# Optimization experiments

Hardware: AMD Instinct MI355X
Metric: run time of the kernel (lower is better)

Reference implementation:

```python
import jax, jax.numpy as jnp
import numpy as np

D_MODEL = 2048
NUM_HEADS = 16
D_K = D_MODEL // NUM_HEADS


def _xavier(key, shape):
    # xavier_uniform_ for a (fan_in, fan_out) matrix
    limit = np.sqrt(6.0 / (shape[0] + shape[1]))
    return jax.random.uniform(key, shape, dtype=jnp.float32, minval=-limit, maxval=limit)


def setup_inputs() -> dict:
    key = jax.random.key(0)
    kx, kq, kk, kv, ko = jax.random.split(key, 5)
    x = jax.random.normal(kx, (4, 2048, D_MODEL), dtype=jnp.float32)
    return {
        "x": x,
        "w_q": _xavier(kq, (D_MODEL, D_MODEL)),
        "w_k": _xavier(kk, (D_MODEL, D_MODEL)),
        "w_v": _xavier(kv, (D_MODEL, D_MODEL)),
        "w_o": _xavier(ko, (D_MODEL, D_MODEL)),
    }


def _split_heads(t):
    b, s, _ = t.shape
    return t.reshape(b, s, NUM_HEADS, D_K).transpose(0, 2, 1, 3)  # [b,h,s,dk]


def reference(x, w_q, w_k, w_v, w_o):
    q = _split_heads(x @ w_q)
    k = _split_heads(x @ w_k)
    v = _split_heads(x @ w_v)
    scale = 1.0 / np.sqrt(D_K).astype(np.float32)
    scores = jnp.einsum("bhqd,bhkd->bhqk", q, k) * scale
    attn = jax.nn.softmax(scores, axis=-1)
    out = jnp.einsum("bhqk,bhkd->bhqd", attn, v)  # [b,h,s,dk]
    b, h, s, dk = out.shape
    out = out.transpose(0, 2, 1, 3).reshape(b, s, h * dk)
    return out @ w_o
```

## Files before the change

kernel.cpp:

```cpp
#include <hip/hip_runtime.h>
#include <hip/hip_bf16.h>

typedef __attribute__((ext_vector_type(8))) __bf16 bf16x8;
typedef __attribute__((ext_vector_type(4))) __bf16 bf16x4;
typedef __attribute__((ext_vector_type(4))) float f32x4;
typedef __attribute__((ext_vector_type(16))) float f32x16;
typedef __attribute__((ext_vector_type(8))) unsigned short u16x8;
typedef unsigned short u16;

#define DEVINL static __device__ __forceinline__

namespace {
constexpr int kB = 4;
constexpr int kS = 2048;
constexpr int kDM = 2048;
constexpr int kH = 16;
constexpr int kDK = 128;
constexpr int kM = kB * kS;
constexpr int kNQKV = 3 * kDM;
constexpr float kE2 = 0.08838834764831845f * 1.44269504088896f;
}

DEVINL u16 f2bf(float f) {
  __hip_bfloat16 h = __float2bfloat16(f);
  return __builtin_bit_cast(u16, h);
}

#if __has_builtin(__builtin_amdgcn_exp2f)
DEVINL float exp2_fast(float x) { return __builtin_amdgcn_exp2f(x); }
#else
DEVINL float exp2_fast(float x) { return exp2f(x); }
#endif

#define GLOAD16(gp, lp) \
  __builtin_amdgcn_global_load_lds((const __attribute__((address_space(1))) void*)(gp), \
                                   (__attribute__((address_space(3))) void*)(lp), 16, 0, 0)

DEVINL bf16x8 lds_frag(const u16* p) { return *reinterpret_cast<const bf16x8*>(p); }

DEVINL f32x4 MFMA16x16(bf16x8 a, bf16x8 b, f32x4 c) {
  return __builtin_amdgcn_mfma_f32_16x16x32_bf16(a, b, c, 0, 0, 0);
}

struct TrueT { static constexpr bool value = true; };
struct FalseT { static constexpr bool value = false; };

__global__ __launch_bounds__(256) void cast_x_kernel(const float* __restrict__ x,
                                                     u16* __restrict__ o, int n4) {
  int i = blockIdx.x * 256 + threadIdx.x;
  if (i >= n4) return;
  float4 v = reinterpret_cast<const float4*>(x)[i];
  ushort4 r;
  r.x = f2bf(v.x); r.y = f2bf(v.y); r.z = f2bf(v.z); r.w = f2bf(v.w);
  reinterpret_cast<ushort4*>(o)[i] = r;
}

__global__ __launch_bounds__(256) void transpose_w_kernel(const float* __restrict__ w0,
    const float* __restrict__ w1, const float* __restrict__ w2, const float* __restrict__ w3,
    u16* __restrict__ wtcat, u16* __restrict__ wot) {
  const float* src = (blockIdx.z == 0) ? w0 : (blockIdx.z == 1) ? w1
                    : (blockIdx.z == 2) ? w2 : w3;
  u16* dst = (blockIdx.z < 3) ? (wtcat + (size_t)blockIdx.z * kDM * kDM) : wot;
  __shared__ float tile[32][33];
  int n0 = blockIdx.x * 32, k0 = blockIdx.y * 32;
  int tx = threadIdx.x, ty = threadIdx.y;
#pragma unroll
  for (int i = 0; i < 4; ++i)
    tile[ty + i * 8][tx] = src[(size_t)(k0 + ty + i * 8) * kDM + n0 + tx];
  __syncthreads();
#pragma unroll
  for (int i = 0; i < 4; ++i)
    dst[(size_t)(n0 + ty + i * 8) * kDM + k0 + tx] = f2bf(tile[tx][ty + i * 8]);
}

__global__ __launch_bounds__(256) void transpose_v_kernel(const u16* __restrict__ qkv,
                                                          u16* __restrict__ vt) {
  int bh = blockIdx.z, b = bh >> 4, h = bh & 15;
  int s0 = blockIdx.x * 32, d0 = blockIdx.y * 32;
  __shared__ u16 tile[32][33];
  int tx = threadIdx.x, ty = threadIdx.y;
#pragma unroll
  for (int i = 0; i < 4; ++i)
    tile[ty + i * 8][tx] =
        qkv[(size_t)(b * kS + s0 + ty + i * 8) * kNQKV + 2 * kDM + h * kDK + d0 + tx];
  __syncthreads();
#pragma unroll
  for (int i = 0; i < 4; ++i)
    vt[(size_t)(bh * kDK + d0 + ty + i * 8) * kS + s0 + tx] = tile[tx][ty + i * 8];
}

DEVINL void cstore(float* p, float v) { *p = v; }
DEVINL void cstore(u16* p, float v) { *p = f2bf(v); }

#define BAR_MID()                                      \
  __builtin_amdgcn_sched_barrier(0);                   \
  __builtin_amdgcn_s_barrier();                        \
  asm volatile("s_waitcnt lgkmcnt(0)" ::: "memory");   \
  __builtin_amdgcn_sched_barrier(0);                   \
  __builtin_amdgcn_s_setprio(1)

#define BAR_END()                                      \
  __builtin_amdgcn_s_setprio(0);                       \
  __builtin_amdgcn_sched_barrier(0);                   \
  __builtin_amdgcn_s_barrier()

#define LGK8() asm volatile("s_waitcnt lgkmcnt(8)" ::: "memory")

#define RD_A(SB, MQ)                                                  \
  do {                                                                \
    _Pragma("unroll") for (int mf = 0; mf < 4; ++mf) {                \
      const u16* p_ = (SB) + (awrow + (MQ) * 64 + mf * 16) * 64;      \
      a[mf * 2 + 0] = lds_frag(p_ + g0);                              \
      a[mf * 2 + 1] = lds_frag(p_ + g1);                              \
    }                                                                 \
  } while (0)

#define RD_B(SB, NH)                                                  \
  do {                                                                \
    _Pragma("unroll") for (int nf = 0; nf < 2; ++nf) {                \
      const u16* p_ = (SB) + (bwrow + (NH) * 32 + nf * 16) * 64;      \
      b[(NH) * 4 + nf * 2 + 0] = lds_frag(p_ + g0);                   \
      b[(NH) * 4 + nf * 2 + 1] = lds_frag(p_ + g1);                   \
    }                                                                 \
  } while (0)

#define MM16(MQ, NH)                                                  \
  do {                                                                \
    _Pragma("unroll") for (int mf = 0; mf < 4; ++mf)                  \
      _Pragma("unroll") for (int nf = 0; nf < 2; ++nf) {              \
        f32x4 t_ = acc[(MQ) * 4 + mf][(NH) * 2 + nf];                 \
        t_ = MFMA16x16(a[mf * 2 + 0], b[(NH) * 4 + nf * 2 + 0], t_);  \
        t_ = MFMA16x16(a[mf * 2 + 1], b[(NH) * 4 + nf * 2 + 1], t_);  \
        acc[(MQ) * 4 + mf][(NH) * 2 + nf] = t_;                       \
      }                                                               \
  } while (0)

#define STG_A(buf, R0, kt) \
  GLOAD16(baseA + (size_t)(R0) * lda + (size_t)(kt) * 64, ldsA + (buf) * 16384 + (R0) * 64)
#define STG_B(buf, R0, kt) \
  GLOAD16(baseB + (size_t)(R0) * ldb + (size_t)(kt) * 64, ldsB + (buf) * 16384 + (R0) * 64)

template <typename CT>
__global__ __launch_bounds__(512, 2) void gemm256_kernel(const u16* __restrict__ A,
    const u16* __restrict__ Bt, CT* __restrict__ C, int K, int lda, int ldb, int ldc) {
  __shared__ __align__(16) u16 sA[2][16384];
  __shared__ __align__(16) u16 sB[2][16384];
  const int tid = threadIdx.x;
  const int lane = tid & 63, wid = tid >> 6;
  const int r15 = lane & 15, hi = lane >> 4;
  const int wm = wid >> 2, wn = wid & 3;

  const int gx = gridDim.x, nwg = gx * gridDim.y;
  const int orig = blockIdx.y * gx + blockIdx.x;
  const int wg = (orig & 7) * (nwg >> 3) + (orig >> 3);
  const int n0 = (wg % gx) * 256;
  const int m0 = (wg / gx) * 256;

  const int NT = K >> 6;
  const int NITER = NT >> 1;

  const int rc = tid >> 3;
  const int cg = (tid & 7) ^ (rc & 7);
  const u16* baseA = A + (size_t)(m0 + rc) * lda + cg * 8;
  const u16* baseB = Bt + (size_t)(n0 + rc) * ldb + cg * 8;
  u16* ldsA = &sA[0][0] + rc * 64 + (tid & 7) * 8;
  u16* ldsB = &sB[0][0] + rc * 64 + (tid & 7) * 8;

  const int sw = r15 & 7;
  const int g0 = (hi ^ sw) * 8;
  const int g1 = ((4 + hi) ^ sw) * 8;
  const int awrow = wm * 128 + r15;
  const int bwrow = wn * 64 + r15;
  const u16* sA0 = &sA[0][0]; const u16* sA1 = &sA[1][0];
  const u16* sB0 = &sB[0][0]; const u16* sB1 = &sB[1][0];

  f32x4 acc[8][4] = {};
  bf16x8 a[8], b[8];

  STG_A(0, 0, 0); STG_A(0, 64, 0); STG_A(0, 128, 0); STG_A(0, 192, 0);
  STG_B(0, 0, 0); STG_B(0, 64, 0); STG_B(0, 128, 0); STG_B(0, 192, 0);
  STG_A(1, 0, 1); STG_A(1, 128, 1);
  STG_B(1, 0, 1); STG_B(1, 64, 1); STG_B(1, 128, 1); STG_B(1, 192, 1);
  asm volatile("s_waitcnt vmcnt(6)" ::: "memory");
  __builtin_amdgcn_sched_barrier(0);
  __builtin_amdgcn_s_barrier();

  int kb = 0;
  auto iter = [&](auto lastc) {
    constexpr bool L = decltype(lastc)::value;
    const int kO = kb + 1, k2 = kb + 2, k3 = kb + 3;
    RD_A(sA0, 0); RD_B(sB0, 0);
    STG_A(1, 64, kO); STG_A(1, 192, kO);
    LGK8(); BAR_MID(); MM16(0, 0); BAR_END();
    RD_B(sB0, 1);
    if constexpr (!L) { STG_A(0, 0, k2); STG_A(0, 128, k2); }
    BAR_MID(); MM16(0, 1); BAR_END();
    RD_A(sA0, 1);
    if constexpr (!L) { STG_B(0, 0, k2); STG_B(0, 64, k2); }
    BAR_MID(); MM16(1, 0); BAR_END();
    if constexpr (!L) { STG_B(0, 128, k2); STG_B(0, 192, k2); }
    BAR_MID(); MM16(1, 1);
    __builtin_amdgcn_s_setprio(0);
    if constexpr (L) { asm volatile("s_waitcnt vmcnt(0)" ::: "memory"); }
    else             { asm volatile("s_waitcnt vmcnt(6)" ::: "memory"); }
    __builtin_amdgcn_sched_barrier(0);
    __builtin_amdgcn_s_barrier();
    RD_A(sA1, 0); RD_B(sB1, 0);
    if constexpr (!L) { STG_A(0, 64, k2); STG_A(0, 192, k2); }
    LGK8(); BAR_MID(); MM16(0, 0); BAR_END();
    RD_B(sB1, 1);
    if constexpr (!L) { STG_A(1, 0, k3); STG_A(1, 128, k3); }
    BAR_MID(); MM16(0, 1); BAR_END();
    RD_A(sA1, 1);
    if constexpr (!L) { STG_B(1, 0, k3); STG_B(1, 64, k3); }
    BAR_MID(); MM16(1, 0); BAR_END();
    if constexpr (!L) { STG_B(1, 128, k3); STG_B(1, 192, k3); }
    BAR_MID(); MM16(1, 1);
    __builtin_amdgcn_s_setprio(0);
    if constexpr (L) { asm volatile("s_waitcnt vmcnt(0)" ::: "memory"); }
    else             { asm volatile("s_waitcnt vmcnt(6)" ::: "memory"); }
    __builtin_amdgcn_sched_barrier(0);
    __builtin_amdgcn_s_barrier();
    kb += 2;
  };
  for (int i = 0; i < NITER - 1; ++i) iter(FalseT{});
  iter(TrueT{});

  const size_t crow0 = (size_t)(m0 + wm * 128 + hi * 4);
  const int col0 = n0 + wn * 64 + r15;
#pragma unroll
  for (int im = 0; im < 8; ++im)
#pragma unroll
    for (int in = 0; in < 4; ++in)
#pragma unroll
      for (int r = 0; r < 4; ++r)
        cstore(&C[(crow0 + im * 16 + r) * ldc + col0 + in * 16], acc[im][in][r]);
}

__global__ __launch_bounds__(256, 2) void attn_kernel(const u16* __restrict__ qkv,
    const u16* __restrict__ vt, u16* __restrict__ attn_out) {
  __shared__ __align__(16) u16 lds[2][16384];
  const int tid = threadIdx.x;
  const int lane = tid & 63, wid = tid >> 6;
  const int l31 = lane & 31, hi5 = lane >> 5;
  const int q0 = blockIdx.x * 128, h = blockIdx.y, b = blockIdx.z;
  const int bh = b * kH + h;

  const int krow = tid >> 4, kg = tid & 15;
  const u16* kp = qkv + (size_t)(b * kS + krow) * kNQKV + kDM + h * kDK
                  + (size_t)((kg ^ (krow & 7)) * 8);
  const int vrow = tid >> 3, vg = tid & 7;
  const u16* vp = vt + (size_t)(bh * kDK + vrow) * kS + (size_t)((vg ^ (vrow & 7)) * 8);

  auto stage_kv = [&](u16* dst) {
#pragma unroll
    for (int i = 0; i < 4; ++i)
      GLOAD16(kp + (size_t)i * 16 * kNQKV, dst + (tid + 256 * i) * 8);
#pragma unroll
    for (int i = 0; i < 4; ++i)
      GLOAD16(vp + (size_t)i * 32 * kS, dst + 8192 + (tid + 256 * i) * 8);
    kp += (size_t)64 * kNQKV;
    vp += 64;
  };

#pragma unroll
  for (int i = 0; i < 8; ++i) {
    int row = (tid >> 4) + 16 * i;
    GLOAD16(qkv + (size_t)(b * kS + q0 + row) * kNQKV + h * kDK
                + (size_t)(((tid & 15) ^ (row & 7)) * 8),
            (u16*)lds[1] + (tid + 256 * i) * 8);
  }
  stage_kv(lds[0]);
  __syncthreads();

  bf16x8 qf[8];
  {
    const int qrow = wid * 32 + l31;
    const u16* qb = (const u16*)lds[1];
#pragma unroll
    for (int ds = 0; ds < 8; ++ds) {
      int slot = (ds * 2 + hi5) ^ (qrow & 7);
      qf[ds] = lds_frag(&qb[qrow * 128 + slot * 8]);
    }
  }
  __syncthreads();

  f32x16 o[4] = {};
  float mi = -1e30f, li = 0.f;
  int cur = 0;

  for (int t = 0; t < kS / 64; ++t) {
    if (t < kS / 64 - 1) stage_kv(lds[cur ^ 1]);

    const u16* Kb = (const u16*)lds[cur];
    const u16* Vb = Kb + 8192;

    f32x16 s0 = {}, s1 = {};
    const int kr = l31;
#pragma unroll
    for (int ds = 0; ds < 8; ++ds) {
      int slot = ((ds * 2 + hi5) ^ (kr & 7)) * 8;
      bf16x8 k0 = lds_frag(&Kb[kr * 128 + slot]);
      bf16x8 k1 = lds_frag(&Kb[(32 + kr) * 128 + slot]);
      s0 = __builtin_amdgcn_mfma_f32_32x32x16_bf16(k0, qf[ds], s0, 0, 0, 0);
      s1 = __builtin_amdgcn_mfma_f32_32x32x16_bf16(k1, qf[ds], s1, 0, 0, 0);
    }

    float mx = s0[0];
#pragma unroll
    for (int r = 1; r < 16; ++r) mx = fmaxf(mx, s0[r]);
#pragma unroll
    for (int r = 0; r < 16; ++r) mx = fmaxf(mx, s1[r]);
    mx = fmaxf(mx, __shfl_xor(mx, 32));
    float mc = mx * kE2;
    if (__any(mc > mi + 8.0f)) {
      float mn = fmaxf(mi, mc);
      float corr = exp2_fast(mi - mn);
      mi = mn;
      li *= corr;
#pragma unroll
      for (int r = 0; r < 16; ++r) {
        float c = __shfl(corr, (r & 3) + 8 * (r >> 2) + 4 * hi5);
        o[0][r] *= c; o[1][r] *= c; o[2][r] *= c; o[3][r] *= c;
      }
    }
    float p0[16], p1[16];
    float rs = 0.f;
#pragma unroll
    for (int r = 0; r < 16; ++r) { p0[r] = exp2_fast(s0[r] * kE2 - mi); rs += p0[r]; }
#pragma unroll
    for (int r = 0; r < 16; ++r) { p1[r] = exp2_fast(s1[r] * kE2 - mi); rs += p1[r]; }
    rs += __shfl_xor(rs, 32);
    li += rs;

    u16x8 pw0, pw1, pw2, pw3;
#pragma unroll
    for (int r = 0; r < 8; ++r) {
      pw0[r] = f2bf(p0[r]);
      pw1[r] = f2bf(p0[r + 8]);
      pw2[r] = f2bf(p1[r]);
      pw3[r] = f2bf(p1[r + 8]);
    }
    bf16x8 pa[4] = {__builtin_bit_cast(bf16x8, pw0), __builtin_bit_cast(bf16x8, pw1),
                    __builtin_bit_cast(bf16x8, pw2), __builtin_bit_cast(bf16x8, pw3)};

#pragma unroll
    for (int dt = 0; dt < 4; ++dt) {
      const int row = dt * 32 + l31;
      const int rs8 = row & 7;
#pragma unroll
      for (int ks = 0; ks < 4; ++ks) {
        bf16x4 vlo = *reinterpret_cast<const bf16x4*>(
            &Vb[row * 64 + ((ks * 2) ^ rs8) * 8 + hi5 * 4]);
        bf16x4 vhi = *reinterpret_cast<const bf16x4*>(
            &Vb[row * 64 + ((ks * 2 + 1) ^ rs8) * 8 + hi5 * 4]);
        bf16x8 bv = __builtin_shufflevector(vlo, vhi, 0, 1, 2, 3, 4, 5, 6, 7);
        o[dt] = __builtin_amdgcn_mfma_f32_32x32x16_bf16(pa[ks], bv, o[dt], 0, 0, 0);
      }
    }

    __syncthreads();
    cur ^= 1;
  }

  float rli = 1.0f / li;
  const size_t obase = (size_t)(b * kS + q0 + wid * 32) * kDM + h * kDK + l31;
#pragma unroll
  for (int r = 0; r < 16; ++r) {
    int ql = (r & 3) + 8 * (r >> 2) + 4 * hi5;
    float w = __shfl(rli, ql);
#pragma unroll
    for (int dt = 0; dt < 4; ++dt)
      attn_out[obase + (size_t)ql * kDM + dt * 32] = f2bf(o[dt][r] * w);
  }
}

extern "C" void kernel_launch(void* const* d_in, const int* in_sizes, int n_in,
                              void* d_out, int out_size, void* d_ws, size_t ws_size,
                              hipStream_t stream) {
  (void)in_sizes; (void)n_in; (void)out_size; (void)ws_size;
  const float* x  = (const float*)d_in[0];
  const float* wq = (const float*)d_in[1];
  const float* wk = (const float*)d_in[2];
  const float* wv = (const float*)d_in[3];
  const float* wo = (const float*)d_in[4];

  char* p = (char*)d_ws;
  u16* xb   = (u16*)p; p += (size_t)kM * kDM * 2;
  u16* wtc  = (u16*)p; p += (size_t)kNQKV * kDM * 2;
  u16* wot  = (u16*)p; p += (size_t)kDM * kDM * 2;
  u16* qkvb = (u16*)p; p += (size_t)kM * kNQKV * 2;
  u16* vtb  = (u16*)p; p += (size_t)kB * kH * kDK * kS * 2;
  u16* aob  = xb;

  int n4 = kM * kDM / 4;
  cast_x_kernel<<<(n4 + 255) / 256, 256, 0, stream>>>(x, xb, n4);
  transpose_w_kernel<<<dim3(kDM / 32, kDM / 32, 4), dim3(32, 8), 0, stream>>>(
      wq, wk, wv, wo, wtc, wot);
  gemm256_kernel<u16><<<dim3(kNQKV / 256, kM / 256), 512, 0, stream>>>(
      xb, wtc, qkvb, kDM, kDM, kDM, kNQKV);
  transpose_v_kernel<<<dim3(kS / 32, kDK / 32, kB * kH), dim3(32, 8), 0, stream>>>(
      qkvb, vtb);
  attn_kernel<<<dim3(kS / 128, kH, kB), 256, 0, stream>>>(qkvb, vtb, aob);
  gemm256_kernel<float><<<dim3(kDM / 256, kM / 256), 512, 0, stream>>>(
      aob, wot, (float*)d_out, kDM, kDM, kDM, kDM);
}
```

Baseline: 460.4 us.

## Double-buffer A fragments in registers to overlap LDS reads with MFMA phases

Splits the A register fragments into even and odd sets so each phase issues the LDS reads for the next phase before running its own MFMAs. The first fragments are loaded before the loop, and the global-load wait moves earlier to allow this. The aim is to hide LDS read latency behind matrix math instead of stalling on lgkmcnt before each MFMA block. The extra fragment registers raise register pressure, which could reduce occupancy at launch bounds of 512 threads with 2 blocks, and the reordered waits and barriers risk ordering errors in the shared-memory buffers.

Result: no change. 460.3 us (-0.0%).

```diff
diff --git a/kernel.cpp b/kernel.cpp
--- a/kernel.cpp
+++ b/kernel.cpp
@@ -92,30 +92,42 @@
 DEVINL void cstore(float* p, float v) { *p = v; }
 DEVINL void cstore(u16* p, float v) { *p = f2bf(v); }
 
-#define BAR_MID()                                      \
+#define PH_OPEN()                                      \
   __builtin_amdgcn_sched_barrier(0);                   \
   __builtin_amdgcn_s_barrier();                        \
   asm volatile("s_waitcnt lgkmcnt(0)" ::: "memory");   \
   __builtin_amdgcn_sched_barrier(0);                   \
   __builtin_amdgcn_s_setprio(1)
 
-#define BAR_END()                                      \
+#define PH_CLOSE()                                     \
   __builtin_amdgcn_s_setprio(0);                       \
   __builtin_amdgcn_sched_barrier(0);                   \
   __builtin_amdgcn_s_barrier()
 
-#define LGK8() asm volatile("s_waitcnt lgkmcnt(8)" ::: "memory")
-
-#define RD_A(SB, MQ)                                                  \
+#define PH_CLOSE_G4()                                  \
+  __builtin_amdgcn_s_setprio(0);                       \
+  __builtin_amdgcn_sched_barrier(0);                   \
+  asm volatile("s_waitcnt vmcnt(4)" ::: "memory");     \
+  __builtin_amdgcn_sched_barrier(0);                   \
+  __builtin_amdgcn_s_barrier()
+
+#define PH_CLOSE_G0()                                  \
+  __builtin_amdgcn_s_setprio(0);                       \
+  __builtin_amdgcn_sched_barrier(0);                   \
+  asm volatile("s_waitcnt vmcnt(0)" ::: "memory");     \
+  __builtin_amdgcn_sched_barrier(0);                   \
+  __builtin_amdgcn_s_barrier()
+
+#define RD_A(SB, MQ, DST)                                             \
   do {                                                                \
     _Pragma("unroll") for (int mf = 0; mf < 4; ++mf) {                \
       const u16* p_ = (SB) + (awrow + (MQ) * 64 + mf * 16) * 64;      \
-      a[mf * 2 + 0] = lds_frag(p_ + g0);                              \
-      a[mf * 2 + 1] = lds_frag(p_ + g1);                              \
+      DST[mf * 2 + 0] = lds_frag(p_ + g0);                            \
+      DST[mf * 2 + 1] = lds_frag(p_ + g1);                            \
     }                                                                 \
   } while (0)
 
-#define RD_B(SB, NH)                                                  \
+#define RD_BH(SB, NH)                                                 \
   do {                                                                \
     _Pragma("unroll") for (int nf = 0; nf < 2; ++nf) {                \
       const u16* p_ = (SB) + (bwrow + (NH) * 32 + nf * 16) * 64;      \
@@ -124,13 +136,13 @@
     }                                                                 \
   } while (0)
 
-#define MM16(MQ, NH)                                                  \
+#define MMQ(MQ, NH, AF)                                               \
   do {                                                                \
     _Pragma("unroll") for (int mf = 0; mf < 4; ++mf)                  \
       _Pragma("unroll") for (int nf = 0; nf < 2; ++nf) {              \
         f32x4 t_ = acc[(MQ) * 4 + mf][(NH) * 2 + nf];                 \
-        t_ = MFMA16x16(a[mf * 2 + 0], b[(NH) * 4 + nf * 2 + 0], t_);  \
-        t_ = MFMA16x16(a[mf * 2 + 1], b[(NH) * 4 + nf * 2 + 1], t_);  \
+        t_ = MFMA16x16(AF[mf * 2 + 0], b[(NH) * 4 + nf * 2 + 0], t_); \
+        t_ = MFMA16x16(AF[mf * 2 + 1], b[(NH) * 4 + nf * 2 + 1], t_); \
         acc[(MQ) * 4 + mf][(NH) * 2 + nf] = t_;                       \
       }                                                               \
   } while (0)
@@ -175,7 +187,7 @@
   const u16* sB0 = &sB[0][0]; const u16* sB1 = &sB[1][0];
 
   f32x4 acc[8][4] = {};
-  bf16x8 a[8], b[8];
+  bf16x8 aE[8], aO[8], b[8];
 
   STG_A(0, 0, 0); STG_A(0, 64, 0); STG_A(0, 128, 0); STG_A(0, 192, 0);
   STG_B(0, 0, 0); STG_B(0, 64, 0); STG_B(0, 128, 0); STG_B(0, 192, 0);
@@ -184,43 +196,50 @@
   asm volatile("s_waitcnt vmcnt(6)" ::: "memory");
   __builtin_amdgcn_sched_barrier(0);
   __builtin_amdgcn_s_barrier();
+  RD_A(sA0, 0, aE); RD_BH(sB0, 0);
 
   int kb = 0;
   auto iter = [&](auto lastc) {
     constexpr bool L = decltype(lastc)::value;
     const int kO = kb + 1, k2 = kb + 2, k3 = kb + 3;
-    RD_A(sA0, 0); RD_B(sB0, 0);
     STG_A(1, 64, kO); STG_A(1, 192, kO);
-    LGK8(); BAR_MID(); MM16(0, 0); BAR_END();
-    RD_B(sB0, 1);
+    PH_OPEN();
+    RD_BH(sB0, 1);
+    MMQ(0, 0, aE);
+    PH_CLOSE();
     if constexpr (!L) { STG_A(0, 0, k2); STG_A(0, 128, k2); }
-    BAR_MID(); MM16(0, 1); BAR_END();
-    RD_A(sA0, 1);
+    PH_OPEN();
+    RD_A(sA0, 1, aO);
+    MMQ(0, 1, aE);
+    PH_CLOSE();
     if constexpr (!L) { STG_B(0, 0, k2); STG_B(0, 64, k2); }
-    BAR_MID(); MM16(1, 0); BAR_END();
+    PH_OPEN();
+    MMQ(1, 0, aO);
+    if constexpr (L) { PH_CLOSE_G0(); } else { PH_CLOSE_G4(); }
     if constexpr (!L) { STG_B(0, 128, k2); STG_B(0, 192, k2); }
-    BAR_MID(); MM16(1, 1);
-    __builtin_amdgcn_s_setprio(0);
-    if constexpr (L) { asm volatile("s_waitcnt vmcnt(0)" ::: "memory"); }
-    else             { asm volatile("s_waitcnt vmcnt(6)" ::: "memory"); }
-    __builtin_amdgcn_sched_barrier(0);
-    __builtin_amdgcn_s_barrier();
-    RD_A(sA1, 0); RD_B(sB1, 0);
+    PH_OPEN();
+    RD_A(sA1, 0, aE); RD_BH(sB1, 0);
+    MMQ(1, 1, aO);
+    PH_CLOSE();
     if constexpr (!L) { STG_A(0, 64, k2); STG_A(0, 192, k2); }
-    LGK8(); BAR_MID(); MM16(0, 0); BAR_END();
-    RD_B(sB1, 1);
+    PH_OPEN();
+    RD_BH(sB1, 1);
+    MMQ(0, 0, aE);
+    PH_CLOSE();
     if constexpr (!L) { STG_A(1, 0, k3); STG_A(1, 128, k3); }
-    BAR_MID(); MM16(0, 1); BAR_END();
-    RD_A(sA1, 1);
+    PH_OPEN();
+    RD_A(sA1, 1, aO);
+    MMQ(0, 1, aE);
+    PH_CLOSE();
     if constexpr (!L) { STG_B(1, 0, k3); STG_B(1, 64, k3); }
-    BAR_MID(); MM16(1, 0); BAR_END();
+    PH_OPEN();
+    MMQ(1, 0, aO);
+    if constexpr (L) { PH_CLOSE_G0(); } else { PH_CLOSE_G4(); }
     if constexpr (!L) { STG_B(1, 128, k3); STG_B(1, 192, k3); }
-    BAR_MID(); MM16(1, 1);
-    __builtin_amdgcn_s_setprio(0);
-    if constexpr (L) { asm volatile("s_waitcnt vmcnt(0)" ::: "memory"); }
-    else             { asm volatile("s_waitcnt vmcnt(6)" ::: "memory"); }
-    __builtin_amdgcn_sched_barrier(0);
-    __builtin_amdgcn_s_barrier();
+    PH_OPEN();
+    if constexpr (!L) { RD_A(sA0, 0, aE); RD_BH(sB0, 0); }
+    MMQ(1, 1, aO);
+    PH_CLOSE();
     kb += 2;
   };
   for (int i = 0; i < NITER - 1; ++i) iter(FalseT{});
```
